# Optimization experiments

Hardware: AMD Instinct MI355X
Metric: run time of the kernel (lower is better)

## Reference

```python
import jax, jax.numpy as jnp
import numpy as np
import math

B, T, N_EMBD, HEAD_SIZE = 8, 2048, 768, 128


def setup_inputs() -> dict:
    key = jax.random.key(0)
    ks = jax.random.split(key, 7)
    s = 0.02
    return {
        "x": jax.random.normal(ks[0], (B, T, N_EMBD), dtype=jnp.float32),
        "Wq": jax.random.normal(ks[1], (N_EMBD, HEAD_SIZE), dtype=jnp.float32) * s,
        "bq": jax.random.normal(ks[2], (HEAD_SIZE,), dtype=jnp.float32) * s,
        "Wk": jax.random.normal(ks[3], (N_EMBD, HEAD_SIZE), dtype=jnp.float32) * s,
        "bk": jax.random.normal(ks[4], (HEAD_SIZE,), dtype=jnp.float32) * s,
        "Wv": jax.random.normal(ks[5], (N_EMBD, HEAD_SIZE), dtype=jnp.float32) * s,
        "bv": jax.random.normal(ks[6], (HEAD_SIZE,), dtype=jnp.float32) * s,
    }


def reference(x, Wq, bq, Wk, bk, Wv, bv):
    # x: [B, T, n_embd]
    Tlen = x.shape[1]
    q = x @ Wq + bq  # [B, T, hs]
    k = x @ Wk + bk
    v = x @ Wv + bv
    scores = jnp.einsum('bqd,bkd->bqk', q, k)  # [B, T, T]
    causal = jnp.tril(jnp.ones((Tlen, Tlen), dtype=bool))
    # original masks with -inf first, then divides by sqrt(head_size); -inf/scale == -inf,
    # so mask-then-scale is mathematically identical.
    scores = jnp.where(causal, scores, -jnp.inf) / math.sqrt(q.shape[-1])
    weights = jax.nn.softmax(scores, axis=-1)
    # dropout p=0.0 (inference/reference) -> identity
    out = jnp.einsum('bqk,bkd->bqd', weights, v)  # [B, T, hs]
    return out
```

## Files before the change

kernel.cpp:

```cpp
#include <hip/hip_runtime.h>

#define B_ 8
#define T_ 2048
#define E_ 768
#define D_ 128
#define SCALE 0.08838834764831845f

typedef _Float16 h8 __attribute__((ext_vector_type(8)));
typedef _Float16 h4 __attribute__((ext_vector_type(4)));
typedef float f4 __attribute__((ext_vector_type(4)));

typedef __attribute__((address_space(1))) unsigned int as1_u32;
typedef __attribute__((address_space(3))) unsigned int as3_u32;

__device__ __forceinline__ void gl_lds16(const void* g, void* l) {
    __builtin_amdgcn_global_load_lds((const as1_u32*)g, (as3_u32*)l, 16, 0, 0);
}

__global__ __launch_bounds__(256) void w_prep(
    const float* __restrict__ Wq, const float* __restrict__ Wk,
    const float* __restrict__ Wv, _Float16* __restrict__ Wh)
{
    __shared__ float tile[64][129];
    const int y = blockIdx.x / 12, kc = blockIdx.x % 12;
    const float* W = (y == 0) ? Wq : (y == 1) ? Wk : Wv;
    const int k0 = kc * 64, t = threadIdx.x;
#pragma unroll
    for (int i = 0; i < 32; ++i) {
        const int idx = i * 256 + t;
        tile[idx >> 7][idx & 127] = W[(size_t)(k0 + (idx >> 7)) * D_ + (idx & 127)];
    }
    __syncthreads();
    const int n = t >> 1, hf = t & 1;
#pragma unroll
    for (int j = 0; j < 4; ++j) {
        const int kk = hf * 32 + j * 8;
        h8 hv;
#pragma unroll
        for (int e = 0; e < 8; ++e) hv[e] = (_Float16)tile[kk + e][n];
        *(h8*)&Wh[(size_t)(y * 128 + n) * E_ + k0 + kk] = hv;
    }
}

__global__ __launch_bounds__(256) void qkv_fused(
    const float* __restrict__ x, const _Float16* __restrict__ Wh,
    const float* __restrict__ bq, const float* __restrict__ bk,
    const float* __restrict__ bv,
    _Float16* __restrict__ Qh, _Float16* __restrict__ Kh,
    _Float16* __restrict__ Vt)
{
    __shared__ _Float16 As[64 * 64];
    __shared__ _Float16 Bs[384 * 64];

    const int t = threadIdx.x;
    const int lane = t & 63, w = t >> 6;
    const int quad = lane >> 4, col = lane & 15;
    const int m0 = blockIdx.x * 64;

    f4 acc[4][6];
#pragma unroll
    for (int mt = 0; mt < 4; ++mt)
#pragma unroll
        for (int nt = 0; nt < 6; ++nt) acc[mt][nt] = (f4){0.f, 0.f, 0.f, 0.f};

    const int brl = lane >> 3, bc = lane & 7;

    for (int kb = 0; kb < E_; kb += 64) {
        {
            const int r = t >> 2, cb = (t & 3) * 16;
            const float* xr = &x[(size_t)(m0 + r) * E_ + kb + cb];
#pragma unroll
            for (int i = 0; i < 4; ++i) {
                const float4 v = *(const float4*)(xr + 4 * i);
                h4 hv; hv[0] = (_Float16)v.x; hv[1] = (_Float16)v.y;
                hv[2] = (_Float16)v.z; hv[3] = (_Float16)v.w;
                const int kk4 = cb + 4 * i;
                *(h4*)&As[r * 64 + (((kk4 >> 3) ^ (r & 7)) << 3) + (kk4 & 7)] = hv;
            }
        }
#pragma unroll
        for (int i = 0; i < 12; ++i) {
            const int R = w * 96 + i * 8;
            const int r = R + brl;
            gl_lds16(Wh + (size_t)r * E_ + kb + 8 * (bc ^ (r & 7)), &Bs[R * 64]);
        }
        __syncthreads();

#pragma unroll
        for (int ks = 0; ks < 2; ++ks) {
            const int sc = ((ks << 2) + quad) ^ (col & 7);
            h8 a[4], bf[6];
#pragma unroll
            for (int mt = 0; mt < 4; ++mt)
                a[mt] = *(const h8*)&As[(mt * 16 + col) * 64 + (sc << 3)];
#pragma unroll
            for (int nt = 0; nt < 6; ++nt)
                bf[nt] = *(const h8*)&Bs[(w * 96 + nt * 16 + col) * 64 + (sc << 3)];
#pragma unroll
            for (int mt = 0; mt < 4; ++mt)
#pragma unroll
                for (int nt = 0; nt < 6; ++nt)
                    acc[mt][nt] = __builtin_amdgcn_mfma_f32_16x16x32_f16(
                        a[mt], bf[nt], acc[mt][nt], 0, 0, 0);
        }
        __syncthreads();
    }

    const float* bp[3] = {bq, bk, bv};
    _Float16* Cs = Bs;
#pragma unroll
    for (int nt = 0; nt < 6; ++nt) {
        const int n16 = w * 96 + nt * 16;
        const int y = n16 >> 7, nl = n16 & 127;
        const float bb = bp[y][nl + col];
#pragma unroll
        for (int mt = 0; mt < 4; ++mt)
#pragma unroll
            for (int reg = 0; reg < 4; ++reg) {
                const int m = mt * 16 + quad * 4 + reg;
                Cs[m * 384 + n16 + col] = (_Float16)(acc[mt][nt][reg] + bb);
            }
    }
    __syncthreads();

    {
        const int m = t >> 2, seg = t & 3;
#pragma unroll
        for (int j = 0; j < 8; ++j) {
            const int n = seg * 64 + j * 8;
            const h8 v = *(const h8*)&Cs[m * 384 + n];
            if (n < 128) *(h8*)&Qh[(size_t)(m0 + m) * D_ + n] = v;
            else         *(h8*)&Kh[(size_t)(m0 + m) * D_ + (n - 128)] = v;
        }
    }
    {
        const int vn = t & 127, part = t >> 7;
        const int bidx = m0 >> 11, tt0 = m0 & 2047;
#pragma unroll
        for (int j = 0; j < 4; ++j) {
            const int ms = part * 32 + j * 8;
            h8 hv;
#pragma unroll
            for (int e = 0; e < 8; ++e) hv[e] = Cs[(ms + e) * 384 + 256 + vn];
            *(h8*)&Vt[((size_t)bidx * D_ + vn) * T_ + tt0 + ms] = hv;
        }
    }
}

__global__ __launch_bounds__(256, 2) void flash_attn(
    const _Float16* __restrict__ Qh,
    const _Float16* __restrict__ Kh,
    const _Float16* __restrict__ Vt,
    float* __restrict__ out)
{
    __shared__ __align__(16) char smem[74752];
    _Float16* Ks = (_Float16*)smem;
    _Float16* Vs = (_Float16*)(smem + 32768);
    _Float16* PlB = (_Float16*)(smem + 65536);

    const int t = threadIdx.x, lane = t & 63, w = t >> 6;
    const int quad = lane >> 4, col = lane & 15;
    const int id = blockIdx.x;
    const int b = id & 7;
    const int k6 = id >> 3;
    const int j32 = (k6 < 32) ? (63 - k6) : (k6 - 32);
    const int qbase = j32 * 32;
    const int qw = w & 1, kp = w >> 1;
    const int qrow0 = qbase + qw * 16;
    const int nk = (j32 >> 1) + 1;

    h8 qf[4];
    const _Float16* Qp = Qh + ((size_t)b * T_ + qrow0 + col) * D_ + quad * 8;
#pragma unroll
    for (int ks = 0; ks < 4; ++ks) qf[ks] = *(const h8*)(Qp + ks * 32);
    asm volatile("s_waitcnt vmcnt(0)" ::: "memory");

    f4 o[8];
#pragma unroll
    for (int i = 0; i < 8; ++i) o[i] = (f4){0.f, 0.f, 0.f, 0.f};
    float m_st[4], l_st[4];
#pragma unroll
    for (int r = 0; r < 4; ++r) { m_st[r] = -1e30f; l_st[r] = 0.f; }

    const _Float16* Kb = Kh + (size_t)b * T_ * D_;
    const _Float16* Vb = Vt + (size_t)b * D_ * T_;
    const int krl = lane >> 4, kc = lane & 15;
    const int vrl = lane >> 3, vc = lane & 7;

    auto stage = [&](int buf, int kbase) __attribute__((always_inline)) {
        _Float16* KsB = Ks + buf * 8192;
        _Float16* VsB = Vs + buf * 8192;
#pragma unroll
        for (int i = 0; i < 4; ++i) {
            const int R = w * 16 + i * 4;
            const int r = R + krl;
            gl_lds16(Kb + (size_t)(kbase + r) * D_ + 8 * (kc ^ (r & 7)), KsB + R * D_);
        }
#pragma unroll
        for (int i = 0; i < 4; ++i) {
            const int R = w * 32 + i * 8;
            const int d = R + vrl;
            gl_lds16(Vb + (size_t)d * T_ + kbase + 8 * (vc ^ (d & 7)), VsB + R * 64);
        }
    };

    _Float16* Pw = PlB + w * 1152;

    auto step = [&](int ti, int buf, bool mask) __attribute__((always_inline)) {
        const _Float16* KsB = Ks + buf * 8192;
        const _Float16* VsB = Vs + buf * 8192;
        const int cx = col & 7;

        f4 s[4];
#pragma unroll
        for (int nt = 0; nt < 4; ++nt) s[nt] = (f4){0.f, 0.f, 0.f, 0.f};
        __builtin_amdgcn_s_setprio(1);
#pragma unroll
        for (int nt = 0; nt < 4; ++nt) {
            const int r = nt * 16 + col;
#pragma unroll
            for (int ks = 0; ks < 4; ++ks) {
                const h8 kf = *(const h8*)(KsB + r * D_ + 8 * (((ks << 2) + quad) ^ cx));
                s[nt] = __builtin_amdgcn_mfma_f32_16x16x32_f16(qf[ks], kf, s[nt], 0, 0, 0);
            }
        }
        __builtin_amdgcn_s_setprio(0);

        if (mask) {
#pragma unroll
            for (int nt = 0; nt < 4; ++nt) {
                const int key = ti * 64 + nt * 16 + col;
#pragma unroll
                for (int reg = 0; reg < 4; ++reg) {
                    const int qr = qrow0 + quad * 4 + reg;
                    const float sv = s[nt][reg] * SCALE;
                    s[nt][reg] = (key <= qr) ? sv : -1e30f;
                }
            }
        } else {
#pragma unroll
            for (int nt = 0; nt < 4; ++nt)
#pragma unroll
                for (int reg = 0; reg < 4; ++reg) s[nt][reg] *= SCALE;
        }

        float mloc[4];
#pragma unroll
        for (int reg = 0; reg < 4; ++reg)
            mloc[reg] = fmaxf(fmaxf(s[0][reg], s[1][reg]), fmaxf(s[2][reg], s[3][reg]));
#pragma unroll
        for (int off = 1; off < 16; off <<= 1)
#pragma unroll
            for (int reg = 0; reg < 4; ++reg)
                mloc[reg] = fmaxf(mloc[reg], __shfl_xor(mloc[reg], off));

        float alpha[4];
#pragma unroll
        for (int reg = 0; reg < 4; ++reg) {
            const float mn = fmaxf(m_st[reg], mloc[reg]);
            alpha[reg] = __expf(m_st[reg] - mn);
            m_st[reg] = mn;
        }
        float rs[4] = {0.f, 0.f, 0.f, 0.f};
#pragma unroll
        for (int nt = 0; nt < 4; ++nt)
#pragma unroll
            for (int reg = 0; reg < 4; ++reg) {
                const float p = __expf(s[nt][reg] - m_st[reg]);
                s[nt][reg] = p;
                rs[reg] += p;
            }
#pragma unroll
        for (int off = 1; off < 16; off <<= 1)
#pragma unroll
            for (int reg = 0; reg < 4; ++reg) rs[reg] += __shfl_xor(rs[reg], off);
#pragma unroll
        for (int reg = 0; reg < 4; ++reg) l_st[reg] = l_st[reg] * alpha[reg] + rs[reg];

#pragma unroll
        for (int n2 = 0; n2 < 8; ++n2)
#pragma unroll
            for (int reg = 0; reg < 4; ++reg) o[n2][reg] *= alpha[reg];

#pragma unroll
        for (int nt = 0; nt < 4; ++nt)
#pragma unroll
            for (int reg = 0; reg < 4; ++reg)
                Pw[(quad * 4 + reg) * 72 + nt * 16 + col] = (_Float16)s[nt][reg];
        const h8 pa0 = *(const h8*)(Pw + col * 72 + quad * 8);
        const h8 pa1 = *(const h8*)(Pw + col * 72 + 32 + quad * 8);

        __builtin_amdgcn_s_setprio(1);
#pragma unroll
        for (int n2 = 0; n2 < 8; ++n2) {
            const int d = n2 * 16 + col;
            const h8 vf0 = *(const h8*)(VsB + d * 64 + 8 * (quad ^ cx));
            const h8 vf1 = *(const h8*)(VsB + d * 64 + 8 * ((4 + quad) ^ cx));
            o[n2] = __builtin_amdgcn_mfma_f32_16x16x32_f16(pa0, vf0, o[n2], 0, 0, 0);
            o[n2] = __builtin_amdgcn_mfma_f32_16x16x32_f16(pa1, vf1, o[n2], 0, 0, 0);
        }
        __builtin_amdgcn_s_setprio(0);
    };

    stage(0, 0);
    for (int ti = 0; ti < nk; ++ti) {
        const int cur = ti & 1;
        if (ti + 1 < nk) {
            stage(cur ^ 1, (ti + 1) << 6);
            asm volatile("s_waitcnt vmcnt(8)" ::: "memory");
        } else {
            asm volatile("s_waitcnt vmcnt(0)" ::: "memory");
        }
        __builtin_amdgcn_s_barrier();
        asm volatile("" ::: "memory");
        if ((ti & 1) == kp) step(ti, cur, ti == nk - 1);
        asm volatile("" ::: "memory");
        __builtin_amdgcn_s_barrier();
        asm volatile("" ::: "memory");
    }

    float* Os = (float*)smem;
    float* Mx = (float*)(smem + 16384);
    float* Lx = Mx + 32;

    __syncthreads();
    if (kp == 1) {
#pragma unroll
        for (int reg = 0; reg < 4; ++reg) {
            const int row = qw * 16 + quad * 4 + reg;
            if (col == 0) { Mx[row] = m_st[reg]; Lx[row] = l_st[reg]; }
#pragma unroll
            for (int n2 = 0; n2 < 8; ++n2)
                Os[row * D_ + n2 * 16 + col] = o[n2][reg];
        }
    }
    __syncthreads();
    if (kp == 0) {
#pragma unroll
        for (int reg = 0; reg < 4; ++reg) {
            const int row = qw * 16 + quad * 4 + reg;
            const float m1 = Mx[row], l1 = Lx[row];
            const float mN = fmaxf(m_st[reg], m1);
            const float a0 = __expf(m_st[reg] - mN);
            const float a1 = __expf(m1 - mN);
            const float inv = 1.0f / (l_st[reg] * a0 + l1 * a1);
#pragma unroll
            for (int n2 = 0; n2 < 8; ++n2) {
                const float v = (o[n2][reg] * a0 + Os[row * D_ + n2 * 16 + col] * a1) * inv;
                out[((size_t)b * T_ + qbase + row) * D_ + n2 * 16 + col] = v;
            }
        }
    }
}

extern "C" void kernel_launch(void* const* d_in, const int* in_sizes, int n_in,
                              void* d_out, int out_size, void* d_ws, size_t ws_size,
                              hipStream_t stream) {
    const float* x  = (const float*)d_in[0];
    const float* Wq = (const float*)d_in[1];
    const float* bq = (const float*)d_in[2];
    const float* Wk = (const float*)d_in[3];
    const float* bk = (const float*)d_in[4];
    const float* Wv = (const float*)d_in[5];
    const float* bv = (const float*)d_in[6];

    _Float16* Qh = (_Float16*)d_ws;
    _Float16* Kh = Qh + (size_t)B_ * T_ * D_;
    _Float16* Vt = Kh + (size_t)B_ * T_ * D_;
    _Float16* Wh = (_Float16*)d_out;

    w_prep<<<dim3(36), dim3(256), 0, stream>>>(Wq, Wk, Wv, Wh);
    qkv_fused<<<dim3(B_ * T_ / 64), dim3(256), 0, stream>>>(
        x, Wh, bq, bk, bv, Qh, Kh, Vt);
    flash_attn<<<dim3(512), dim3(256), 0, stream>>>(Qh, Kh, Vt, (float*)d_out);
}
```

Baseline: 177.5 us.

## Double-buffer QKV GEMM and split attention key tiles across warp halves

The QKV projection kernel now double-buffers the A and B LDS tiles. The next x chunk is prefetched into registers and the next W chunk is staged while the current chunk's MFMAs run, which removes the load-then-sync serialization. In flash attention, each warp pair now handles half of every 64-key tile (32 keys each) instead of alternating whole tiles, and fully masked halves on the diagonal are skipped. The O/l rescale is applied only when some row max grows, and the block ordering is simplified to descending query tiles. The cost is more LDS in the GEMM, which may lower occupancy, plus a wave-wide branch in the softmax.

```diff
diff --git a/kernel.cpp b/kernel.cpp
--- a/kernel.cpp
+++ b/kernel.cpp
@@ -49,8 +49,8 @@
     _Float16* __restrict__ Qh, _Float16* __restrict__ Kh,
     _Float16* __restrict__ Vt)
 {
-    __shared__ _Float16 As[64 * 64];
-    __shared__ _Float16 Bs[384 * 64];
+    __shared__ _Float16 As[2][64 * 64];
+    __shared__ _Float16 Bs[2][384 * 64];
 
     const int t = threadIdx.x;
     const int lane = t & 63, w = t >> 6;
@@ -64,38 +64,53 @@
         for (int nt = 0; nt < 6; ++nt) acc[mt][nt] = (f4){0.f, 0.f, 0.f, 0.f};
 
     const int brl = lane >> 3, bc = lane & 7;
-
-    for (int kb = 0; kb < E_; kb += 64) {
-        {
-            const int r = t >> 2, cb = (t & 3) * 16;
-            const float* xr = &x[(size_t)(m0 + r) * E_ + kb + cb];
-#pragma unroll
-            for (int i = 0; i < 4; ++i) {
-                const float4 v = *(const float4*)(xr + 4 * i);
-                h4 hv; hv[0] = (_Float16)v.x; hv[1] = (_Float16)v.y;
-                hv[2] = (_Float16)v.z; hv[3] = (_Float16)v.w;
-                const int kk4 = cb + 4 * i;
-                *(h4*)&As[r * 64 + (((kk4 >> 3) ^ (r & 7)) << 3) + (kk4 & 7)] = hv;
-            }
-        }
-#pragma unroll
-        for (int i = 0; i < 12; ++i) {
-            const int R = w * 96 + i * 8;
-            const int r = R + brl;
-            gl_lds16(Wh + (size_t)r * E_ + kb + 8 * (bc ^ (r & 7)), &Bs[R * 64]);
-        }
-        __syncthreads();
-
+    const int xr_ = t >> 2, xcb = (t & 3) * 16;
+
+    float4 xv[4];
+
+#define LOAD_X(kb)                                                          \
+    {   const float* xr = &x[(size_t)(m0 + xr_) * E_ + (kb) + xcb];         \
+        _Pragma("unroll")                                                   \
+        for (int i = 0; i < 4; ++i) xv[i] = *(const float4*)(xr + 4 * i);   }
+
+#define STAGE_B(dst, kb)                                                    \
+    _Pragma("unroll")                                                       \
+    for (int i = 0; i < 12; ++i) {                                          \
+        const int R = w * 96 + i * 8;                                       \
+        const int r = R + brl;                                              \
+        gl_lds16(Wh + (size_t)r * E_ + (kb) + 8 * (bc ^ (r & 7)), &(dst)[R * 64]); }
+
+#define WRITE_A(dst)                                                        \
+    _Pragma("unroll")                                                       \
+    for (int i = 0; i < 4; ++i) {                                           \
+        h4 hv; hv[0] = (_Float16)xv[i].x; hv[1] = (_Float16)xv[i].y;        \
+        hv[2] = (_Float16)xv[i].z; hv[3] = (_Float16)xv[i].w;               \
+        const int kk4 = xcb + 4 * i;                                        \
+        *(h4*)&(dst)[xr_ * 64 + (((kk4 >> 3) ^ (xr_ & 7)) << 3) + (kk4 & 7)] = hv; }
+
+    LOAD_X(0);
+    STAGE_B(Bs[0], 0);
+    asm volatile("s_waitcnt vmcnt(12)" ::: "memory");
+    WRITE_A(As[0]);
+    __syncthreads();
+
+#pragma unroll 2
+    for (int it = 0; it < 12; ++it) {
+        const int c = it & 1;
+        if (it < 11) {
+            LOAD_X((it + 1) * 64);
+            STAGE_B(Bs[c ^ 1], (it + 1) * 64);
+        }
 #pragma unroll
         for (int ks = 0; ks < 2; ++ks) {
             const int sc = ((ks << 2) + quad) ^ (col & 7);
             h8 a[4], bf[6];
 #pragma unroll
             for (int mt = 0; mt < 4; ++mt)
-                a[mt] = *(const h8*)&As[(mt * 16 + col) * 64 + (sc << 3)];
+                a[mt] = *(const h8*)&As[c][(mt * 16 + col) * 64 + (sc << 3)];
 #pragma unroll
             for (int nt = 0; nt < 6; ++nt)
-                bf[nt] = *(const h8*)&Bs[(w * 96 + nt * 16 + col) * 64 + (sc << 3)];
+                bf[nt] = *(const h8*)&Bs[c][(w * 96 + nt * 16 + col) * 64 + (sc << 3)];
 #pragma unroll
             for (int mt = 0; mt < 4; ++mt)
 #pragma unroll
@@ -103,11 +118,15 @@
                     acc[mt][nt] = __builtin_amdgcn_mfma_f32_16x16x32_f16(
                         a[mt], bf[nt], acc[mt][nt], 0, 0, 0);
         }
+        if (it < 11) {
+            asm volatile("s_waitcnt vmcnt(12)" ::: "memory");
+            WRITE_A(As[c ^ 1]);
+        }
         __syncthreads();
     }
 
     const float* bp[3] = {bq, bk, bv};
-    _Float16* Cs = Bs;
+    _Float16* Cs = &Bs[0][0];
 #pragma unroll
     for (int nt = 0; nt < 6; ++nt) {
         const int n16 = w * 96 + nt * 16;
@@ -145,6 +164,9 @@
             *(h8*)&Vt[((size_t)bidx * D_ + vn) * T_ + tt0 + ms] = hv;
         }
     }
+#undef LOAD_X
+#undef STAGE_B
+#undef WRITE_A
 }
 
 __global__ __launch_bounds__(256, 2) void flash_attn(
@@ -153,19 +175,18 @@
     const _Float16* __restrict__ Vt,
     float* __restrict__ out)
 {
-    __shared__ __align__(16) char smem[74752];
+    __shared__ __align__(16) char smem[70656];
     _Float16* Ks = (_Float16*)smem;
     _Float16* Vs = (_Float16*)(smem + 32768);
-    _Float16* PlB = (_Float16*)(smem + 65536);
+    _Float16* Pb = (_Float16*)(smem + 65536);
 
     const int t = threadIdx.x, lane = t & 63, w = t >> 6;
     const int quad = lane >> 4, col = lane & 15;
     const int id = blockIdx.x;
     const int b = id & 7;
-    const int k6 = id >> 3;
-    const int j32 = (k6 < 32) ? (63 - k6) : (k6 - 32);
+    const int j32 = 63 - (id >> 3);
+    const int qw = w & 1, kh = w >> 1;
     const int qbase = j32 * 32;
-    const int qw = w & 1, kp = w >> 1;
     const int qrow0 = qbase + qw * 16;
     const int nk = (j32 >> 1) + 1;
 
@@ -186,6 +207,7 @@
     const _Float16* Vb = Vt + (size_t)b * D_ * T_;
     const int krl = lane >> 4, kc = lane & 15;
     const int vrl = lane >> 3, vc = lane & 7;
+    const int cx = col & 7;
 
     auto stage = [&](int buf, int kbase) __attribute__((always_inline)) {
         _Float16* KsB = Ks + buf * 8192;
@@ -204,20 +226,19 @@
         }
     };
 
-    _Float16* Pw = PlB + w * 1152;
+    _Float16* Pw = Pb + w * 640;
 
     auto step = [&](int ti, int buf, bool mask) __attribute__((always_inline)) {
         const _Float16* KsB = Ks + buf * 8192;
         const _Float16* VsB = Vs + buf * 8192;
-        const int cx = col & 7;
-
-        f4 s[4];
-#pragma unroll
-        for (int nt = 0; nt < 4; ++nt) s[nt] = (f4){0.f, 0.f, 0.f, 0.f};
+
+        f4 s[2];
+        s[0] = (f4){0.f, 0.f, 0.f, 0.f};
+        s[1] = (f4){0.f, 0.f, 0.f, 0.f};
         __builtin_amdgcn_s_setprio(1);
 #pragma unroll
-        for (int nt = 0; nt < 4; ++nt) {
-            const int r = nt * 16 + col;
+        for (int nt = 0; nt < 2; ++nt) {
+            const int r = kh * 32 + nt * 16 + col;
 #pragma unroll
             for (int ks = 0; ks < 4; ++ks) {
                 const h8 kf = *(const h8*)(KsB + r * D_ + 8 * (((ks << 2) + quad) ^ cx));
@@ -228,8 +249,8 @@
 
         if (mask) {
 #pragma unroll
-            for (int nt = 0; nt < 4; ++nt) {
-                const int key = ti * 64 + nt * 16 + col;
+            for (int nt = 0; nt < 2; ++nt) {
+                const int key = ti * 64 + kh * 32 + nt * 16 + col;
 #pragma unroll
                 for (int reg = 0; reg < 4; ++reg) {
                     const int qr = qrow0 + quad * 4 + reg;
@@ -239,31 +260,37 @@
             }
         } else {
 #pragma unroll
-            for (int nt = 0; nt < 4; ++nt)
+            for (int nt = 0; nt < 2; ++nt)
 #pragma unroll
                 for (int reg = 0; reg < 4; ++reg) s[nt][reg] *= SCALE;
         }
 
         float mloc[4];
 #pragma unroll
-        for (int reg = 0; reg < 4; ++reg)
-            mloc[reg] = fmaxf(fmaxf(s[0][reg], s[1][reg]), fmaxf(s[2][reg], s[3][reg]));
+        for (int reg = 0; reg < 4; ++reg) mloc[reg] = fmaxf(s[0][reg], s[1][reg]);
 #pragma unroll
         for (int off = 1; off < 16; off <<= 1)
 #pragma unroll
             for (int reg = 0; reg < 4; ++reg)
                 mloc[reg] = fmaxf(mloc[reg], __shfl_xor(mloc[reg], off));
 
-        float alpha[4];
-#pragma unroll
-        for (int reg = 0; reg < 4; ++reg) {
-            const float mn = fmaxf(m_st[reg], mloc[reg]);
-            alpha[reg] = __expf(m_st[reg] - mn);
-            m_st[reg] = mn;
-        }
+        bool grow = (mloc[0] > m_st[0]) | (mloc[1] > m_st[1]) |
+                    (mloc[2] > m_st[2]) | (mloc[3] > m_st[3]);
+        if (__any((int)grow)) {
+#pragma unroll
+            for (int reg = 0; reg < 4; ++reg) {
+                const float mn = fmaxf(m_st[reg], mloc[reg]);
+                const float alpha = __expf(m_st[reg] - mn);
+                m_st[reg] = mn;
+                l_st[reg] *= alpha;
+#pragma unroll
+                for (int n2 = 0; n2 < 8; ++n2) o[n2][reg] *= alpha;
+            }
+        }
+
         float rs[4] = {0.f, 0.f, 0.f, 0.f};
 #pragma unroll
-        for (int nt = 0; nt < 4; ++nt)
+        for (int nt = 0; nt < 2; ++nt)
 #pragma unroll
             for (int reg = 0; reg < 4; ++reg) {
                 const float p = __expf(s[nt][reg] - m_st[reg]);
@@ -275,34 +302,27 @@
 #pragma unroll
             for (int reg = 0; reg < 4; ++reg) rs[reg] += __shfl_xor(rs[reg], off);
 #pragma unroll
-        for (int reg = 0; reg < 4; ++reg) l_st[reg] = l_st[reg] * alpha[reg] + rs[reg];
-
-#pragma unroll
-        for (int n2 = 0; n2 < 8; ++n2)
-#pragma unroll
-            for (int reg = 0; reg < 4; ++reg) o[n2][reg] *= alpha[reg];
-
-#pragma unroll
-        for (int nt = 0; nt < 4; ++nt)
+        for (int reg = 0; reg < 4; ++reg) l_st[reg] += rs[reg];
+
+#pragma unroll
+        for (int nt = 0; nt < 2; ++nt)
 #pragma unroll
             for (int reg = 0; reg < 4; ++reg)
-                Pw[(quad * 4 + reg) * 72 + nt * 16 + col] = (_Float16)s[nt][reg];
-        const h8 pa0 = *(const h8*)(Pw + col * 72 + quad * 8);
-        const h8 pa1 = *(const h8*)(Pw + col * 72 + 32 + quad * 8);
+                Pw[(quad * 4 + reg) * 40 + nt * 16 + col] = (_Float16)s[nt][reg];
+        const h8 pa = *(const h8*)(Pw + col * 40 + quad * 8);
 
         __builtin_amdgcn_s_setprio(1);
 #pragma unroll
         for (int n2 = 0; n2 < 8; ++n2) {
             const int d = n2 * 16 + col;
-            const h8 vf0 = *(const h8*)(VsB + d * 64 + 8 * (quad ^ cx));
-            const h8 vf1 = *(const h8*)(VsB + d * 64 + 8 * ((4 + quad) ^ cx));
-            o[n2] = __builtin_amdgcn_mfma_f32_16x16x32_f16(pa0, vf0, o[n2], 0, 0, 0);
-            o[n2] = __builtin_amdgcn_mfma_f32_16x16x32_f16(pa1, vf1, o[n2], 0, 0, 0);
+            const h8 vf = *(const h8*)(VsB + d * 64 + 8 * ((kh * 4 + quad) ^ (d & 7)));
+            o[n2] = __builtin_amdgcn_mfma_f32_16x16x32_f16(pa, vf, o[n2], 0, 0, 0);
         }
         __builtin_amdgcn_s_setprio(0);
     };
 
     stage(0, 0);
+    const bool evenJ = ((j32 & 1) == 0);
     for (int ti = 0; ti < nk; ++ti) {
         const int cur = ti & 1;
         if (ti + 1 < nk) {
@@ -312,11 +332,12 @@
             asm volatile("s_waitcnt vmcnt(0)" ::: "memory");
         }
         __builtin_amdgcn_s_barrier();
-        asm volatile("" ::: "memory");
-        if ((ti & 1) == kp) step(ti, cur, ti == nk - 1);
-        asm volatile("" ::: "memory");
+        const bool last = (ti == nk - 1);
+        if (!(last && evenJ && kh == 1)) {
+            const bool mask = last && (kh == (j32 & 1));
+            step(ti, cur, mask);
+        }
         __builtin_amdgcn_s_barrier();
-        asm volatile("" ::: "memory");
     }
 
     float* Os = (float*)smem;
@@ -324,7 +345,7 @@
     float* Lx = Mx + 32;
 
     __syncthreads();
-    if (kp == 1) {
+    if (kh == 1) {
 #pragma unroll
         for (int reg = 0; reg < 4; ++reg) {
             const int row = qw * 16 + quad * 4 + reg;
@@ -335,7 +356,7 @@
         }
     }
     __syncthreads();
-    if (kp == 0) {
+    if (kh == 0) {
 #pragma unroll
         for (int reg = 0; reg < 4; ++reg) {
             const int row = qw * 16 + quad * 4 + reg;
```

New measurement: 173.4 us. 2.3% less time.
